# Performance work log

Hardware: AMD Instinct MI355X
Metric: run time of the kernel (lower is better)

Reference implementation:

```python
import jax, jax.numpy as jnp
import numpy as np

B = 512
IN_FEATURES = 512
OUT_FEATURES = 100
KERNEL_DIM = 5


def setup_inputs() -> dict:
    key = jax.random.key(0)
    kx, kT = jax.random.split(key)
    x = jax.random.normal(kx, (B, IN_FEATURES), dtype=jnp.float32)
    # nn.init.normal_(T, 0, 1)
    T = jax.random.normal(kT, (IN_FEATURES, OUT_FEATURES, KERNEL_DIM), dtype=jnp.float32)
    return {"x": x, "T": T}


def reference(x, T):
    # matrices = x @ T.view(in, out*k) -> (B, out, k)
    M = jnp.einsum('bi,iok->bok', x, T)  # [B, O, K]
    # pairwise L1 distance over kernel dim: norm[i, j, o] = sum_k |M[i,o,k] - M[j,o,k]|
    norm = jnp.abs(M[:, None, :, :] - M[None, :, :, :]).sum(-1)  # [B, B, O]
    expnorm = jnp.exp(-norm)
    # sum over first batch axis; subtract 1 to remove self-term (exp(0) = 1)
    o_b = expnorm.sum(0) - 1.0  # [B, O]
    return o_b
```

## Files before the change

### kernel.cpp

```cpp
#include <hip/hip_runtime.h>
#include <math.h>


#define NB    512
#define NIN   512
#define NOUT  100
#define KDIM  5
#define NCOL  500
#define LOG2E 1.44269504088896340736f

__global__ __launch_bounds__(256) void gemm_kernel(const float* __restrict__ A,
                                                   const float* __restrict__ Tg,
                                                   float* __restrict__ M8o) {
    __shared__ float As[64][72];
    __shared__ float Pr[4][64][8];

    const int itile = blockIdx.x;
    const int o     = blockIdx.y;
    const int t     = threadIdx.x;
    const int lane  = t & 63;
    const int cq    = __builtin_amdgcn_readfirstlane(t >> 6);

    const float* To = Tg + o * KDIM;

    float acc[5] = {0.f, 0.f, 0.f, 0.f, 0.f};

    for (int ct = 0; ct < 8; ++ct) {
        __syncthreads();
        #pragma unroll
        for (int l = 0; l < 4; ++l) {
            const int idx = t + l * 256;
            const int row = idx >> 4, q = idx & 15;
            *reinterpret_cast<float4*>(&As[row][q * 4]) =
                *reinterpret_cast<const float4*>(
                    &A[(itile * 64 + row) * NIN + ct * 64 + q * 4]);
        }
        __syncthreads();

        const int cb = ct * 64 + cq * 16;
        #pragma unroll
        for (int cc = 0; cc < 16; cc += 4) {
            const float4 xv = *reinterpret_cast<const float4*>(&As[lane][cq * 16 + cc]);
            const float xr[4] = {xv.x, xv.y, xv.z, xv.w};
            #pragma unroll
            for (int q = 0; q < 4; ++q) {
                const float* tp = To + (cb + cc + q) * NCOL;
                #pragma unroll
                for (int k = 0; k < 5; ++k)
                    acc[k] = fmaf(xr[q], tp[k], acc[k]);
            }
        }
    }

    #pragma unroll
    for (int k = 0; k < 5; ++k) Pr[cq][lane][k] = acc[k];
    __syncthreads();

    if (t < 64) {
        float s[5];
        #pragma unroll
        for (int k = 0; k < 5; ++k)
            s[k] = (Pr[0][t][k] + Pr[1][t][k] + Pr[2][t][k] + Pr[3][t][k]) * LOG2E;
        float* dst = M8o + (o * NB + itile * 64 + t) * 8;
        *reinterpret_cast<float4*>(dst)     = make_float4(s[0], s[1], s[2], s[3]);
        *reinterpret_cast<float4*>(dst + 4) = make_float4(s[4], 0.f, 0.f, 0.f);
    }
}

__global__ __launch_bounds__(256) void pairwise_kernel(const float* __restrict__ M8o,
                                                       float* __restrict__ out) {
    __shared__ float Ms[NB * 8];
    __shared__ float Pw[16][16][4];

    const int o  = blockIdx.x;
    const int jc = blockIdx.y;
    const int t  = threadIdx.x;

    {
        const float4* src = reinterpret_cast<const float4*>(M8o + o * NB * 8);
        float4* dst = reinterpret_cast<float4*>(Ms);
        #pragma unroll
        for (int l = 0; l < 4; ++l) dst[t + l * 256] = src[t + l * 256];
    }
    __syncthreads();

    const int is = t & 15;
    const int jg = t >> 4;
    const int jbase = jc * 64 + jg * 4;

    float jv[4][5];
    #pragma unroll
    for (int jj = 0; jj < 4; ++jj) {
        const float* m = &Ms[(jbase + jj) * 8];
        #pragma unroll
        for (int k = 0; k < 5; ++k) jv[jj][k] = m[k];
    }

    float acc[4] = {0.f, 0.f, 0.f, 0.f};
    #pragma unroll 4
    for (int it = 0; it < 32; ++it) {
        const float* m = &Ms[(it * 16 + is) * 8];
        const float m0 = m[0], m1 = m[1], m2 = m[2], m3 = m[3], m4 = m[4];
        #pragma unroll
        for (int jj = 0; jj < 4; ++jj) {
            const float n = fabsf(m0 - jv[jj][0]) + fabsf(m1 - jv[jj][1])
                          + fabsf(m2 - jv[jj][2]) + fabsf(m3 - jv[jj][3])
                          + fabsf(m4 - jv[jj][4]);
            acc[jj] += exp2f(-n);
        }
    }

    *reinterpret_cast<float4*>(&Pw[is][jg][0]) =
        make_float4(acc[0], acc[1], acc[2], acc[3]);
    __syncthreads();

    if (t < 64) {
        const int g = t >> 2, jj = t & 3;
        float tot = -1.0f;
        #pragma unroll
        for (int s = 0; s < 16; ++s) tot += Pw[s][g][jj];
        out[(jc * 64 + g * 4 + jj) * NOUT + o] = tot;
    }
}

extern "C" void kernel_launch(void* const* d_in, const int* in_sizes, int n_in,
                              void* d_out, int out_size, void* d_ws, size_t ws_size,
                              hipStream_t stream) {
    const float* x = (const float*)d_in[0];
    const float* T = (const float*)d_in[1];
    float* M8o = (float*)d_ws;
    float* out = (float*)d_out;

    gemm_kernel<<<dim3(8, NOUT), 256, 0, stream>>>(x, T, M8o);
    pairwise_kernel<<<dim3(NOUT, 8), 256, 0, stream>>>(M8o, out);
}
```

Measured before the change: 85.45 us.

## Fuse projection GEMM and pairwise kernel into one per-output-feature kernel

Replaces the two-kernel pipeline (GEMM writing M to workspace, then pairwise exp-L1 reduction) with a single kernel. Each block stages one output feature's T slice in LDS, recomputes all 512 rows of M for that feature, then does the pairwise reduction over 128 columns. This removes the workspace round-trip and a launch. In exchange, each of the 4 column blocks per feature redundantly recomputes the full GEMM for that feature, reading x from global memory per thread.

```diff
diff --git a/kernel.cpp b/kernel.cpp
--- a/kernel.cpp
+++ b/kernel.cpp
@@ -9,117 +9,94 @@
 #define NCOL  500
 #define LOG2E 1.44269504088896340736f
 
-__global__ __launch_bounds__(256) void gemm_kernel(const float* __restrict__ A,
-                                                   const float* __restrict__ Tg,
-                                                   float* __restrict__ M8o) {
-    __shared__ float As[64][72];
-    __shared__ float Pr[4][64][8];
-
-    const int itile = blockIdx.x;
-    const int o     = blockIdx.y;
-    const int t     = threadIdx.x;
-    const int lane  = t & 63;
-    const int cq    = __builtin_amdgcn_readfirstlane(t >> 6);
-
-    const float* To = Tg + o * KDIM;
-
-    float acc[5] = {0.f, 0.f, 0.f, 0.f, 0.f};
-
-    for (int ct = 0; ct < 8; ++ct) {
-        __syncthreads();
-        #pragma unroll
-        for (int l = 0; l < 4; ++l) {
-            const int idx = t + l * 256;
-            const int row = idx >> 4, q = idx & 15;
-            *reinterpret_cast<float4*>(&As[row][q * 4]) =
-                *reinterpret_cast<const float4*>(
-                    &A[(itile * 64 + row) * NIN + ct * 64 + q * 4]);
-        }
-        __syncthreads();
-
-        const int cb = ct * 64 + cq * 16;
-        #pragma unroll
-        for (int cc = 0; cc < 16; cc += 4) {
-            const float4 xv = *reinterpret_cast<const float4*>(&As[lane][cq * 16 + cc]);
-            const float xr[4] = {xv.x, xv.y, xv.z, xv.w};
-            #pragma unroll
-            for (int q = 0; q < 4; ++q) {
-                const float* tp = To + (cb + cc + q) * NCOL;
-                #pragma unroll
-                for (int k = 0; k < 5; ++k)
-                    acc[k] = fmaf(xr[q], tp[k], acc[k]);
-            }
-        }
-    }
-
-    #pragma unroll
-    for (int k = 0; k < 5; ++k) Pr[cq][lane][k] = acc[k];
-    __syncthreads();
-
-    if (t < 64) {
-        float s[5];
-        #pragma unroll
-        for (int k = 0; k < 5; ++k)
-            s[k] = (Pr[0][t][k] + Pr[1][t][k] + Pr[2][t][k] + Pr[3][t][k]) * LOG2E;
-        float* dst = M8o + (o * NB + itile * 64 + t) * 8;
-        *reinterpret_cast<float4*>(dst)     = make_float4(s[0], s[1], s[2], s[3]);
-        *reinterpret_cast<float4*>(dst + 4) = make_float4(s[4], 0.f, 0.f, 0.f);
-    }
-}
-
-__global__ __launch_bounds__(256) void pairwise_kernel(const float* __restrict__ M8o,
-                                                       float* __restrict__ out) {
+__global__ __launch_bounds__(512) void fused_kernel(const float* __restrict__ x,
+                                                    const float* __restrict__ T,
+                                                    float* __restrict__ out) {
+    __shared__ float Tl[KDIM][NB];
     __shared__ float Ms[NB * 8];
-    __shared__ float Pw[16][16][4];
+    __shared__ float Pw[4][128];
 
     const int o  = blockIdx.x;
     const int jc = blockIdx.y;
     const int t  = threadIdx.x;
 
     {
-        const float4* src = reinterpret_cast<const float4*>(M8o + o * NB * 8);
-        float4* dst = reinterpret_cast<float4*>(Ms);
+        const float* src = T + t * NCOL + o * KDIM;
         #pragma unroll
-        for (int l = 0; l < 4; ++l) dst[t + l * 256] = src[t + l * 256];
+        for (int k = 0; k < KDIM; ++k)
+            Tl[k][t] = src[k] * LOG2E;
     }
     __syncthreads();
 
-    const int is = t & 15;
-    const int jg = t >> 4;
-    const int jbase = jc * 64 + jg * 4;
+    {
+        const int cs = t & 1;
+        const int i0 = t & ~1;
+        const float* xr0 = x + i0 * NIN + cs * 256;
+        const float* xr1 = xr0 + NIN;
 
-    float jv[4][5];
-    #pragma unroll
-    for (int jj = 0; jj < 4; ++jj) {
-        const float* m = &Ms[(jbase + jj) * 8];
+        float acc0[5] = {0.f,0.f,0.f,0.f,0.f};
+        float acc1[5] = {0.f,0.f,0.f,0.f,0.f};
+
+        #pragma unroll 2
+        for (int c = 0; c < 256; c += 4) {
+            const float4 xa = *reinterpret_cast<const float4*>(xr0 + c);
+            const float4 xb = *reinterpret_cast<const float4*>(xr1 + c);
+            const int cg = cs * 256 + c;
+            float4 tk[5];
+            #pragma unroll
+            for (int k = 0; k < 5; ++k)
+                tk[k] = *reinterpret_cast<const float4*>(&Tl[k][cg]);
+            const float xa_[4] = {xa.x, xa.y, xa.z, xa.w};
+            const float xb_[4] = {xb.x, xb.y, xb.z, xb.w};
+            #pragma unroll
+            for (int q = 0; q < 4; ++q) {
+                #pragma unroll
+                for (int k = 0; k < 5; ++k) {
+                    const float tv = reinterpret_cast<const float*>(&tk[k])[q];
+                    acc0[k] = fmaf(xa_[q], tv, acc0[k]);
+                    acc1[k] = fmaf(xb_[q], tv, acc1[k]);
+                }
+            }
+        }
         #pragma unroll
-        for (int k = 0; k < 5; ++k) jv[jj][k] = m[k];
-    }
-
-    float acc[4] = {0.f, 0.f, 0.f, 0.f};
-    #pragma unroll 4
-    for (int it = 0; it < 32; ++it) {
-        const float* m = &Ms[(it * 16 + is) * 8];
-        const float m0 = m[0], m1 = m[1], m2 = m[2], m3 = m[3], m4 = m[4];
-        #pragma unroll
-        for (int jj = 0; jj < 4; ++jj) {
-            const float n = fabsf(m0 - jv[jj][0]) + fabsf(m1 - jv[jj][1])
-                          + fabsf(m2 - jv[jj][2]) + fabsf(m3 - jv[jj][3])
-                          + fabsf(m4 - jv[jj][4]);
-            acc[jj] += exp2f(-n);
+        for (int k = 0; k < 5; ++k) {
+            acc0[k] += __shfl_xor(acc0[k], 1, 64);
+            acc1[k] += __shfl_xor(acc1[k], 1, 64);
+        }
+        if (cs == 0) {
+            float* d0 = &Ms[i0 * 8];
+            *reinterpret_cast<float4*>(d0)     = make_float4(acc0[0], acc0[1], acc0[2], acc0[3]);
+            *reinterpret_cast<float4*>(d0 + 4) = make_float4(acc0[4], 0.f, 0.f, 0.f);
+            float* d1 = &Ms[(i0 + 1) * 8];
+            *reinterpret_cast<float4*>(d1)     = make_float4(acc1[0], acc1[1], acc1[2], acc1[3]);
+            *reinterpret_cast<float4*>(d1 + 4) = make_float4(acc1[4], 0.f, 0.f, 0.f);
         }
     }
-
-    *reinterpret_cast<float4*>(&Pw[is][jg][0]) =
-        make_float4(acc[0], acc[1], acc[2], acc[3]);
     __syncthreads();
 
-    if (t < 64) {
-        const int g = t >> 2, jj = t & 3;
-        float tot = -1.0f;
-        #pragma unroll
-        for (int s = 0; s < 16; ++s) tot += Pw[s][g][jj];
-        out[(jc * 64 + g * 4 + jj) * NOUT + o] = tot;
+    {
+        const int jg = t & 127;
+        const int is = t >> 7;
+        const int j  = jc * 128 + jg;
+        const float* mj = &Ms[j * 8];
+        const float jv0 = mj[0], jv1 = mj[1], jv2 = mj[2], jv3 = mj[3], jv4 = mj[4];
+
+        float acc = 0.f;
+        const int ib = is * 128;
+        #pragma unroll 4
+        for (int it = 0; it < 128; ++it) {
+            const float* m = &Ms[(ib + it) * 8];
+            const float n = fabsf(m[0] - jv0) + fabsf(m[1] - jv1) + fabsf(m[2] - jv2)
+                          + fabsf(m[3] - jv3) + fabsf(m[4] - jv4);
+            acc += exp2f(-n);
+        }
+        Pw[is][jg] = acc;
+    }
+    __syncthreads();
+
+    if (t < 128) {
+        const float tot = Pw[0][t] + Pw[1][t] + Pw[2][t] + Pw[3][t] - 1.0f;
+        out[(jc * 128 + t) * NOUT + o] = tot;
     }
 }
 
@@ -128,9 +105,7 @@
                               hipStream_t stream) {
     const float* x = (const float*)d_in[0];
     const float* T = (const float*)d_in[1];
-    float* M8o = (float*)d_ws;
     float* out = (float*)d_out;
 
-    gemm_kernel<<<dim3(8, NOUT), 256, 0, stream>>>(x, T, M8o);
-    pairwise_kernel<<<dim3(NOUT, 8), 256, 0, stream>>>(M8o, out);
+    fused_kernel<<<dim3(NOUT, 4), 512, 0, stream>>>(x, T, out);
 }
```

New measurement: 172.7 us. +102.2%, slower.
